# Kernel tuning notes

Measured on AMD Instinct MI355X. Metric: run time of the kernel, lower is better.

Reference implementation:

```python
import jax, jax.numpy as jnp
import numpy as np

B, T, C, H, D = 8, 2048, 1024, 1024, 4  # batch, seq_len, input_size, hidden_size, dilation


def setup_inputs() -> dict:
    key = jax.random.key(0)
    k1, k2, k3, k4, k5 = jax.random.split(key, 5)
    s = 1.0 / np.sqrt(H).astype(np.float32)  # match nn.LSTM uniform(-1/sqrt(H),1/sqrt(H)) scale
    return {
        "x": jax.random.normal(k1, (B, T, C), jnp.float32),
        "W_ih": jax.random.normal(k2, (4 * H, C), jnp.float32) * s,
        "W_hh": jax.random.normal(k3, (4 * H, H), jnp.float32) * s,
        "b_ih": jax.random.normal(k4, (4 * H,), jnp.float32) * s,
        "b_hh": jax.random.normal(k5, (4 * H,), jnp.float32) * s,
    }


def _dilated_lstm(x, W_ih, W_hh, b_ih, b_hh):
    Bv, Tv, Cv = x.shape
    Tp = -(-Tv // D) * D          # ceil(T/D)*D, static
    L = Tp // D                   # sub-sequence length per dilation phase
    xp = jnp.pad(x, ((0, 0), (0, Tp - Tv), (0, 0)))
    # (B, L, D, C) -> (B, D, L, C) -> (B*D, L, C): D parallel strided slices
    xr = xp.reshape(Bv, L, D, Cv).transpose(0, 2, 1, 3).reshape(Bv * D, L, Cv)
    # Precompute input contribution to all gates once (big GEMM, hoisted out of scan)
    xg = jnp.einsum('blc,gc->blg', xr, W_ih) + b_ih + b_hh  # (B*D, L, 4H)

    h0 = jnp.zeros((Bv * D, H), x.dtype)
    c0 = jnp.zeros((Bv * D, H), x.dtype)

    def step(carry, g_t):
        h, c = carry
        g = g_t + h @ W_hh.T                    # (B*D, 4H), torch gate order i,f,g,o
        i, f, gg, o = jnp.split(g, 4, axis=-1)
        i = jax.nn.sigmoid(i)
        f = jax.nn.sigmoid(f)
        gg = jnp.tanh(gg)
        o = jax.nn.sigmoid(o)
        c = f * c + i * gg
        h = o * jnp.tanh(c)
        return (h, c), h

    _, ys = jax.lax.scan(step, (h0, c0), xg.transpose(1, 0, 2))  # ys: (L, B*D, H)
    y = ys.transpose(1, 0, 2)                                    # (B*D, L, H)
    y = y.reshape(Bv, D, L, H).transpose(0, 2, 1, 3).reshape(Bv, Tp, H)
    return y[:, :Tv, :]


def reference(x, W_ih, W_hh, b_ih, b_hh):
    return _dilated_lstm(x, W_ih, W_hh, b_ih, b_hh)
```

## Files before the change

### kernel.cpp

```cpp
#include <hip/hip_runtime.h>
#include <cstdint>

typedef __attribute__((ext_vector_type(8))) _Float16 half8;
typedef __attribute__((ext_vector_type(4))) _Float16 half4;
typedef __attribute__((ext_vector_type(4))) float f32x4;
typedef unsigned short u16;
typedef unsigned int u32;
typedef unsigned long long u64;

#define MFMA16F(a, b, c) __builtin_amdgcn_mfma_f32_16x16x32_f16((a), (b), (c), 0, 0, 0)
#define AGENT __HIP_MEMORY_SCOPE_AGENT

template <int AUX>
__device__ __forceinline__ void gl_lds16_a(const void* g, void* lds) {
  __builtin_amdgcn_global_load_lds(
      (const __attribute__((address_space(1))) unsigned*)g,
      (__attribute__((address_space(3))) unsigned*)lds, 16, 0, AUX);
}

__device__ __forceinline__ float sigm(float x) { return 1.f / (1.f + __expf(-x)); }
__device__ __forceinline__ float tanh_f(float x) { return 2.f / (1.f + __expf(-2.f * x)) - 1.f; }

__global__ void k_cvt(const float* __restrict__ in, _Float16* __restrict__ o, int n4) {
  int i = blockIdx.x * blockDim.x + threadIdx.x;
  int stride = gridDim.x * blockDim.x;
  for (; i < n4; i += stride) {
    float4 v = ((const float4*)in)[i];
    half4 h = {(_Float16)v.x, (_Float16)v.y, (_Float16)v.z, (_Float16)v.w};
    ((half4*)o)[i] = h;
  }
}

__global__ void k_bias(const float* __restrict__ bi, const float* __restrict__ bh,
                       float* __restrict__ bias) {
  int i = blockIdx.x * blockDim.x + threadIdx.x;
  if (i < 4096) bias[i] = bi[i] + bh[i];
}

__global__ void k_init4(u64* __restrict__ hf) {
  const int i = blockIdx.x * blockDim.x + threadIdx.x;
  const u64 v = (i < 8192) ? 0ull : 0x0001000100010001ull;
  __hip_atomic_store(&hf[i], v, __ATOMIC_RELAXED, AGENT);
}

__global__ __launch_bounds__(256) void k_gemm1(
    const u16* __restrict__ Aw, const u16* __restrict__ Bw,
    const float* __restrict__ bias, _Float16* __restrict__ xg) {
  __shared__ u16 sA[4096];
  __shared__ u16 sB[4096];
  const int tid = threadIdx.x, lane = tid & 63, wid = tid >> 6;
  const int bm = blockIdx.x >> 5, bn = blockIdx.x & 31;
  const int m0 = bm * 128, n0 = bn * 128;
  const int wr = wid >> 1, wc = wid & 1;
  f32x4 acc[4][4] = {};

  for (int kt = 0; kt < 32; ++kt) {
#pragma unroll
    for (int rb = 0; rb < 2; ++rb) {
      const int base = (rb * 4 + wid) * 1024;
      const int b = base + lane * 16;
      const int row = b >> 6;
      const int q = lane & 3;
      const int sq = ((q - row) & 3) << 4;
      gl_lds16_a<0>((const char*)Aw + (size_t)(m0 + row) * 2048 + (size_t)kt * 64 + sq,
                    (char*)&sA[0] + base);
      gl_lds16_a<0>((const char*)Bw + (size_t)(n0 + row) * 2048 + (size_t)kt * 64 + sq,
                    (char*)&sB[0] + base);
    }
    __syncthreads();
    half8 ah[4], bh[4];
#pragma unroll
    for (int i = 0; i < 4; ++i) {
      const int ra = wr * 64 + i * 16 + (lane & 15);
      ah[i] = *(const half8*)((const char*)sA + ra * 64 + ((((lane >> 4) + ra) & 3) << 4));
      const int rb2 = wc * 64 + i * 16 + (lane & 15);
      bh[i] = *(const half8*)((const char*)sB + rb2 * 64 + ((((lane >> 4) + rb2) & 3) << 4));
    }
#pragma unroll
    for (int i = 0; i < 4; ++i)
#pragma unroll
      for (int j = 0; j < 4; ++j) acc[i][j] = MFMA16F(ah[i], bh[j], acc[i][j]);
    __syncthreads();
  }

#pragma unroll
  for (int j = 0; j < 4; ++j) {
    const int gcol = n0 + wc * 64 + j * 16 + (lane & 15);
    const int gate = gcol >> 10, jj = gcol & 1023;
    const float bv = bias[gcol];
#pragma unroll
    for (int i = 0; i < 4; ++i)
#pragma unroll
      for (int q = 0; q < 4; ++q) {
        const int m = m0 + wr * 64 + i * 16 + (lane >> 4) * 4 + q;
        const int b = m >> 11, t = m & 2047;
        const int s = (b << 2) | (t & 3);
        const int l = t >> 2;
        xg[(((size_t)(l * 32 + s)) * 1024 + jj) * 4 + gate] = (_Float16)(acc[i][j][q] + bv);
      }
  }
}

__global__ __launch_bounds__(512, 1) void k_scan(
    const u16* __restrict__ Whh16, const _Float16* __restrict__ xg,
    u16* __restrict__ hfrag, float* __restrict__ out) {
  const int b = blockIdx.x;
  const int gr = b & 7;
  if (gr >= 4) return;
  const int wl = b >> 3;
  const int tid = threadIdx.x;

  __shared__ u16 h_lds[2][8192];
  const int lane = tid & 63, wid = tid >> 6;
  const int j0 = wl * 32;

  half8 wf[32];
  {
    const int p = lane & 15;
    const int gate = p >> 2, c = p & 3;
    const int koff = (lane >> 4) * 8;
    const size_t rowbase = (size_t)(gate * 1024 + j0 + wid * 4 + c) * 1024;
#pragma unroll
    for (int ks = 0; ks < 32; ++ks) {
      wf[ks] = *(const half8*)(Whh16 + rowbase + ks * 32 + koff);
      asm volatile("" : "+v"(wf[ks]));
    }
  }

  const int m = ((lane >> 4) << 2) | ((lane >> 2) & 3);
  const int jl = (wid << 2) | (lane & 3);
  const int s = gr * 8 + m;
  const int j = j0 + jl;
  float c_reg = 0.f;
  const int hq = wl * 64 + (wid >> 1) * 16 + m * 2 + (wid & 1);

  const u64 M = 0x0001000100010001ull;
  int mode = 0;

  float x0 = 0.f, x1 = 0.f, x2 = 0.f, x3 = 0.f;
  if (lane < 32) {
    const half4 xv = *(const half4*)(xg + ((size_t)s * 1024 + j) * 4);
    x0 = (float)xv[0]; x1 = (float)xv[1]; x2 = (float)xv[2]; x3 = (float)xv[3];
  }

  for (int l = 0; l < 512; ++l) {
    const char* hsrc = (const char*)hfrag + (size_t)(l & 3) * 65536 + gr * 16384;
    u64* hdst = (u64*)((char*)hfrag + (size_t)((l + 1) & 3) * 65536 + gr * 16384);
    const u64 expv = ((l >> 2) & 1) ? M : 0ull;
    const u32 pw = (u32)(((l + 1) >> 2) & 1);
    u16* ldsb = &h_lds[l & 1][0];

    {
      int tries = 0;
      for (;;) {
        if (mode == 0) {
#pragma unroll
          for (int r = 0; r < 2; ++r)
            gl_lds16_a<1>(hsrc + wid * 2048 + r * 1024 + lane * 16,
                          (char*)ldsb + wid * 2048 + r * 1024);
        } else {
#pragma unroll
          for (int r = 0; r < 2; ++r)
            gl_lds16_a<17>(hsrc + wid * 2048 + r * 1024 + lane * 16,
                           (char*)ldsb + wid * 2048 + r * 1024);
        }
        asm volatile("s_waitcnt vmcnt(0)" ::: "memory");
        bool ok = true;
#pragma unroll
        for (int r = 0; r < 2; ++r) {
          const u64* q = (const u64*)((const char*)ldsb + wid * 2048 + r * 1024 + lane * 16);
          ok = ok & (((q[0] ^ expv) & M) == 0) & (((q[1] ^ expv) & M) == 0);
        }
        if (__all(ok)) break;
        if (++tries > 64) mode = 1;
      }
    }
    __syncthreads();

    f32x4 a0 = {0.f, 0.f, 0.f, 0.f}, a1 = a0, a2 = a0, a3 = a0;
    const char* ab = (const char*)ldsb + (lane >> 4) * 128 + (lane & 7) * 16;
#pragma unroll
    for (int ks = 0; ks < 32; ks += 4) {
      const char* cb = ab + ks * 512;
      a0 = MFMA16F(*(const half8*)(cb), wf[ks], a0);
      a1 = MFMA16F(*(const half8*)(cb + 512), wf[ks + 1], a1);
      a2 = MFMA16F(*(const half8*)(cb + 1024), wf[ks + 2], a2);
      a3 = MFMA16F(*(const half8*)(cb + 1536), wf[ks + 3], a3);
    }
    float G0 = (a0[0] + a1[0]) + (a2[0] + a3[0]);
    float G1 = (a0[1] + a1[1]) + (a2[1] + a3[1]);
    float G2 = (a0[2] + a1[2]) + (a2[2] + a3[2]);
    float G3 = (a0[3] + a1[3]) + (a2[3] + a3[3]);

    {
      const bool h2 = (lane & 4) != 0;
      float x, y;
      x = h2 ? G0 : G1; y = __shfl_xor(x, 4);
      G0 = h2 ? y : G0; G1 = h2 ? G1 : y;
      x = h2 ? G2 : G3; y = __shfl_xor(x, 4);
      G2 = h2 ? y : G2; G3 = h2 ? G3 : y;
    }
    {
      const bool h3 = (lane & 8) != 0;
      float x, y;
      x = h3 ? G0 : G2; y = __shfl_xor(x, 8);
      G0 = h3 ? y : G0; G2 = h3 ? G2 : y;
      x = h3 ? G1 : G3; y = __shfl_xor(x, 8);
      G1 = h3 ? y : G1; G3 = h3 ? G3 : y;
    }

    const float gi = G0 + x0, gf = G1 + x1, gg = G2 + x2, go = G3 + x3;
    const float iv = sigm(gi), fv = sigm(gf), gv = tanh_f(gg), ov = sigm(go);
    c_reg = fv * c_reg + iv * gv;
    const float hv = ov * tanh_f(c_reg);

    if (lane < 32) {
      u32 hb = (u32)__builtin_bit_cast(u16, (_Float16)hv);
      hb = (hb & 0xFFFEu) | pw;
      const u32 o1 = (u32)__shfl_xor((int)hb, 1);
      const u32 w1 = (lane & 1) ? ((o1 & 0xFFFFu) | (hb << 16))
                                : ((hb & 0xFFFFu) | (o1 << 16));
      const u32 o2lo = (u32)__shfl_xor((int)w1, 2);
      const u64 v = (lane & 2) ? (((u64)w1 << 32) | (u64)o2lo)
                               : (((u64)o2lo << 32) | (u64)w1);
      if ((lane & 3) == 0)
        __hip_atomic_store(&hdst[hq], v, __ATOMIC_RELAXED, AGENT);

      out[(((size_t)(s >> 2) * 2048) + (size_t)l * 4 + (s & 3)) * 1024 + j] = hv;

      if (l < 511) {
        const half4 xv = *(const half4*)(xg + (((size_t)(l + 1) * 32 + s) * 1024 + j) * 4);
        x0 = (float)xv[0]; x1 = (float)xv[1]; x2 = (float)xv[2]; x3 = (float)xv[3];
      }
    }
  }
}

extern "C" void kernel_launch(void* const* d_in, const int* in_sizes, int n_in,
                              void* d_out, int out_size, void* d_ws, size_t ws_size,
                              hipStream_t stream) {
  const float* x   = (const float*)d_in[0];
  const float* Wih = (const float*)d_in[1];
  const float* Whh = (const float*)d_in[2];
  const float* bih = (const float*)d_in[3];
  const float* bhh = (const float*)d_in[4];
  float* out = (float*)d_out;
  char* ws = (char*)d_ws;

  constexpr size_t OFF_WIH16 = 0;
  constexpr size_t OFF_WHH16 = 8388608;
  constexpr size_t OFF_BIAS  = 16777216;
  constexpr size_t OFF_HFRAG = 16793600;
  constexpr size_t OFF_XG    = 17055744;
  constexpr size_t WS_NEED   = OFF_XG + 134217728;

  if (ws_size < WS_NEED) {
    hipMemsetAsync(d_out, 0, (size_t)out_size * sizeof(float), stream);
    return;
  }

  _Float16* wih16 = (_Float16*)(ws + OFF_WIH16);
  _Float16* whh16 = (_Float16*)(ws + OFF_WHH16);
  float* bias = (float*)(ws + OFF_BIAS);
  u16* hfrag = (u16*)(ws + OFF_HFRAG);
  _Float16* xg = (_Float16*)(ws + OFF_XG);
  _Float16* x16 = (_Float16*)d_out;

  k_cvt<<<1024, 256, 0, stream>>>(Wih, wih16, 4194304 / 4);
  k_cvt<<<1024, 256, 0, stream>>>(Whh, whh16, 4194304 / 4);
  k_cvt<<<2048, 256, 0, stream>>>(x, x16, 16777216 / 4);
  k_bias<<<16, 256, 0, stream>>>(bih, bhh, bias);
  k_init4<<<128, 256, 0, stream>>>((u64*)hfrag);
  k_gemm1<<<4096, 256, 0, stream>>>((const u16*)x16, (const u16*)wih16, bias, xg);
  k_scan<<<256, 512, 0, stream>>>((const u16*)whh16, xg, hfrag, out);
}
```

Baseline: 1.280 ms.

## Use all 256 scan blocks with XCC-aware group assignment via rendezvous

The scan previously launched 256 blocks but used only 128 of them, with each group handling 8 sequences. Now every block runs and each group handles 4 sequences. Each block reads its XCC id and takes a rank through an atomic rendezvous, so the 32 blocks that exchange h-state share one XCC and its L2. This halves the per-step h exchange and LDS footprint per block and keeps inter-block sync traffic on one die, at the cost of a grid-wide spin barrier at startup and reliance on all 256 blocks being co-resident. If the blocks do not split 32 per XCC, it falls back to blockIdx-based mapping with the slower cache mode.

New measurement: 1.272 ms. About the same (-0.6%).

```diff
diff --git a/kernel.cpp b/kernel.cpp
--- a/kernel.cpp
+++ b/kernel.cpp
@@ -37,10 +37,11 @@
   if (i < 4096) bias[i] = bi[i] + bh[i];
 }
 
-__global__ void k_init4(u64* __restrict__ hf) {
+__global__ void k_init4(u64* __restrict__ hf, u32* __restrict__ rdz) {
   const int i = blockIdx.x * blockDim.x + threadIdx.x;
   const u64 v = (i < 8192) ? 0ull : 0x0001000100010001ull;
   __hip_atomic_store(&hf[i], v, __ATOMIC_RELAXED, AGENT);
+  if (i < 16) __hip_atomic_store(&rdz[i], 0u, __ATOMIC_RELAXED, AGENT);
 }
 
 __global__ __launch_bounds__(256) void k_gemm1(
@@ -103,15 +104,32 @@
 
 __global__ __launch_bounds__(512, 1) void k_scan(
     const u16* __restrict__ Whh16, const _Float16* __restrict__ xg,
-    u16* __restrict__ hfrag, float* __restrict__ out) {
+    u16* __restrict__ hfrag, float* __restrict__ out, u32* __restrict__ rdz) {
   const int b = blockIdx.x;
-  const int gr = b & 7;
-  if (gr >= 4) return;
-  const int wl = b >> 3;
   const int tid = threadIdx.x;
-
-  __shared__ u16 h_lds[2][8192];
   const int lane = tid & 63, wid = tid >> 6;
+
+  __shared__ u16 h_lds[2][4096];
+  __shared__ u32 sh_gr, sh_wl, sh_mode;
+
+  if (tid == 0) {
+    u32 my;
+    asm volatile("s_getreg_b32 %0, hwreg(HW_REG_XCC_ID)" : "=s"(my));
+    my &= 7u;
+    const u32 rank = __hip_atomic_fetch_add(&rdz[my], 1u, __ATOMIC_RELAXED, AGENT);
+    __hip_atomic_fetch_add(&rdz[8], 1u, __ATOMIC_RELAXED, AGENT);
+    while (__hip_atomic_load(&rdz[8], __ATOMIC_RELAXED, AGENT) < 256u)
+      __builtin_amdgcn_s_sleep(1);
+    u32 okloc = 1;
+    for (int x = 0; x < 8; ++x)
+      okloc &= (__hip_atomic_load(&rdz[x], __ATOMIC_RELAXED, AGENT) == 32u);
+    sh_gr = okloc ? my : (u32)(b >> 5);
+    sh_wl = okloc ? rank : (u32)(b & 31);
+    sh_mode = okloc ? 0u : 1u;
+  }
+  __syncthreads();
+  const int gr = (int)sh_gr, wl = (int)sh_wl;
+  int mode = (int)sh_mode;
   const int j0 = wl * 32;
 
   half8 wf[32];
@@ -127,25 +145,24 @@
     }
   }
 
-  const int m = ((lane >> 4) << 2) | ((lane >> 2) & 3);
+  const int m = (lane >> 2) & 3;
   const int jl = (wid << 2) | (lane & 3);
-  const int s = gr * 8 + m;
+  const int s = gr * 4 + m;
   const int j = j0 + jl;
   float c_reg = 0.f;
-  const int hq = wl * 64 + (wid >> 1) * 16 + m * 2 + (wid & 1);
+  const int hq = wl * 32 + m * 8 + wid;
 
   const u64 M = 0x0001000100010001ull;
-  int mode = 0;
 
   float x0 = 0.f, x1 = 0.f, x2 = 0.f, x3 = 0.f;
-  if (lane < 32) {
+  if (lane < 16) {
     const half4 xv = *(const half4*)(xg + ((size_t)s * 1024 + j) * 4);
     x0 = (float)xv[0]; x1 = (float)xv[1]; x2 = (float)xv[2]; x3 = (float)xv[3];
   }
 
   for (int l = 0; l < 512; ++l) {
-    const char* hsrc = (const char*)hfrag + (size_t)(l & 3) * 65536 + gr * 16384;
-    u64* hdst = (u64*)((char*)hfrag + (size_t)((l + 1) & 3) * 65536 + gr * 16384);
+    const char* hsrc = (const char*)hfrag + (size_t)(l & 3) * 65536 + gr * 8192;
+    u64* hdst = (u64*)((char*)hfrag + (size_t)((l + 1) & 3) * 65536 + gr * 8192);
     const u64 expv = ((l >> 2) & 1) ? M : 0ull;
     const u32 pw = (u32)(((l + 1) >> 2) & 1);
     u16* ldsb = &h_lds[l & 1][0];
@@ -153,24 +170,13 @@
     {
       int tries = 0;
       for (;;) {
-        if (mode == 0) {
-#pragma unroll
-          for (int r = 0; r < 2; ++r)
-            gl_lds16_a<1>(hsrc + wid * 2048 + r * 1024 + lane * 16,
-                          (char*)ldsb + wid * 2048 + r * 1024);
-        } else {
-#pragma unroll
-          for (int r = 0; r < 2; ++r)
-            gl_lds16_a<17>(hsrc + wid * 2048 + r * 1024 + lane * 16,
-                           (char*)ldsb + wid * 2048 + r * 1024);
-        }
+        if (mode == 0)
+          gl_lds16_a<1>(hsrc + wid * 1024 + lane * 16, (char*)ldsb + wid * 1024);
+        else
+          gl_lds16_a<17>(hsrc + wid * 1024 + lane * 16, (char*)ldsb + wid * 1024);
         asm volatile("s_waitcnt vmcnt(0)" ::: "memory");
-        bool ok = true;
-#pragma unroll
-        for (int r = 0; r < 2; ++r) {
-          const u64* q = (const u64*)((const char*)ldsb + wid * 2048 + r * 1024 + lane * 16);
-          ok = ok & (((q[0] ^ expv) & M) == 0) & (((q[1] ^ expv) & M) == 0);
-        }
+        const u64* q = (const u64*)((const char*)ldsb + wid * 1024 + lane * 16);
+        const bool ok = (((q[0] ^ expv) & M) == 0) & (((q[1] ^ expv) & M) == 0);
         if (__all(ok)) break;
         if (++tries > 64) mode = 1;
       }
@@ -178,14 +184,14 @@
     __syncthreads();
 
     f32x4 a0 = {0.f, 0.f, 0.f, 0.f}, a1 = a0, a2 = a0, a3 = a0;
-    const char* ab = (const char*)ldsb + (lane >> 4) * 128 + (lane & 7) * 16;
+    const char* ab = (const char*)ldsb + (lane & 3) * 64 + (lane >> 4) * 16;
 #pragma unroll
     for (int ks = 0; ks < 32; ks += 4) {
-      const char* cb = ab + ks * 512;
+      const char* cb = ab + ks * 256;
       a0 = MFMA16F(*(const half8*)(cb), wf[ks], a0);
-      a1 = MFMA16F(*(const half8*)(cb + 512), wf[ks + 1], a1);
-      a2 = MFMA16F(*(const half8*)(cb + 1024), wf[ks + 2], a2);
-      a3 = MFMA16F(*(const half8*)(cb + 1536), wf[ks + 3], a3);
+      a1 = MFMA16F(*(const half8*)(cb + 256), wf[ks + 1], a1);
+      a2 = MFMA16F(*(const half8*)(cb + 512), wf[ks + 2], a2);
+      a3 = MFMA16F(*(const half8*)(cb + 768), wf[ks + 3], a3);
     }
     float G0 = (a0[0] + a1[0]) + (a2[0] + a3[0]);
     float G1 = (a0[1] + a1[1]) + (a2[1] + a3[1]);
@@ -214,7 +220,7 @@
     c_reg = fv * c_reg + iv * gv;
     const float hv = ov * tanh_f(c_reg);
 
-    if (lane < 32) {
+    if (lane < 16) {
       u32 hb = (u32)__builtin_bit_cast(u16, (_Float16)hv);
       hb = (hb & 0xFFFEu) | pw;
       const u32 o1 = (u32)__shfl_xor((int)hb, 1);
@@ -251,7 +257,8 @@
   constexpr size_t OFF_WHH16 = 8388608;
   constexpr size_t OFF_BIAS  = 16777216;
   constexpr size_t OFF_HFRAG = 16793600;
-  constexpr size_t OFF_XG    = 17055744;
+  constexpr size_t OFF_RDZ   = 17055744;
+  constexpr size_t OFF_XG    = 17055808;
   constexpr size_t WS_NEED   = OFF_XG + 134217728;
 
   if (ws_size < WS_NEED) {
@@ -263,6 +270,7 @@
   _Float16* whh16 = (_Float16*)(ws + OFF_WHH16);
   float* bias = (float*)(ws + OFF_BIAS);
   u16* hfrag = (u16*)(ws + OFF_HFRAG);
+  u32* rdz = (u32*)(ws + OFF_RDZ);
   _Float16* xg = (_Float16*)(ws + OFF_XG);
   _Float16* x16 = (_Float16*)d_out;
 
@@ -270,7 +278,7 @@
   k_cvt<<<1024, 256, 0, stream>>>(Whh, whh16, 4194304 / 4);
   k_cvt<<<2048, 256, 0, stream>>>(x, x16, 16777216 / 4);
   k_bias<<<16, 256, 0, stream>>>(bih, bhh, bias);
-  k_init4<<<128, 256, 0, stream>>>((u64*)hfrag);
+  k_init4<<<128, 256, 0, stream>>>((u64*)hfrag, rdz);
   k_gemm1<<<4096, 256, 0, stream>>>((const u16*)x16, (const u16*)wih16, bias, xg);
-  k_scan<<<256, 512, 0, stream>>>((const u16*)whh16, xg, hfrag, out);
-}
+  k_scan<<<256, 512, 0, stream>>>((const u16*)whh16, xg, hfrag, out, rdz);
+}
```
